# Performance work log

Hardware: AMD Instinct MI355X
Metric: run time of the kernel (lower is better)

## Reference

```python
import jax, jax.numpy as jnp
import numpy as np

HIDDEN = 64
IN_SIZE = 2048 + 512  # sum(obs_shape) + sum(action_shape)


def setup_inputs() -> dict:
    key = jax.random.key(0)
    ks = jax.random.split(key, 10)
    B = 32768
    s_in = 1.0 / np.sqrt(IN_SIZE)
    s_h = 1.0 / np.sqrt(HIDDEN)
    return {
        "state": jax.random.normal(ks[0], (B, 2048), dtype=jnp.float32),
        "action": jax.random.normal(ks[1], (B, 512), dtype=jnp.float32),
        "hidden_state": jax.random.normal(ks[2], (B, HIDDEN), dtype=jnp.float32),
        "cell_state": jax.random.normal(ks[3], (B, HIDDEN), dtype=jnp.float32),
        # fused gate weights, gate order: [i, f, g, o]
        "Wi": jax.random.uniform(ks[4], (IN_SIZE, 4 * HIDDEN), jnp.float32, -s_in, s_in),
        "bi": jax.random.uniform(ks[5], (4 * HIDDEN,), jnp.float32, -s_in, s_in),
        "Wh": jax.random.uniform(ks[6], (HIDDEN, 4 * HIDDEN), jnp.float32, -s_h, s_h),
        "bh": jax.random.uniform(ks[7], (4 * HIDDEN,), jnp.float32, -s_h, s_h),
        "Wo": jax.random.uniform(ks[8], (HIDDEN, 1), jnp.float32, -s_h, s_h),
        "bo": jax.random.uniform(ks[9], (1,), jnp.float32, -s_h, s_h),
    }


def reference(state, action, hidden_state, cell_state, Wi, bi, Wh, bh, Wo, bo):
    x = jnp.concatenate([state, action], axis=1)  # [B, IN_SIZE]
    # two fused GEMMs covering all 8 Linear layers (gate order i,f,g,o)
    gates = x @ Wi + bi + hidden_state @ Wh + bh  # [B, 4*HIDDEN]
    i_t, f_t, g_t, o_t = jnp.split(gates, 4, axis=1)
    i_t = jax.nn.sigmoid(i_t)
    f_t = jax.nn.sigmoid(f_t)
    g_t = jnp.tanh(g_t)
    o_t = jax.nn.sigmoid(o_t)
    c_t = f_t * cell_state + i_t * g_t
    h_t = o_t * jnp.tanh(c_t)
    out = jnp.tanh(h_t @ Wo + bo)  # [B, 1]
    return (out, h_t, c_t)
```

## Files before the change

kernel.cpp:

```cpp
#include <hip/hip_runtime.h>
#include <hip/hip_bf16.h>

#define K_IN 2624
#define NSTEP 82

typedef __attribute__((ext_vector_type(8))) short short8;
typedef __attribute__((ext_vector_type(4))) float float4_t;

__device__ __forceinline__ short f2bf(float f) {
    union { __hip_bfloat16 b; short s; } u;
    u.b = __float2bfloat16(f);
    return u.s;
}

__device__ __forceinline__ float sigmoid_fast(float x) {
    return 1.f / (1.f + __expf(-x));
}

__device__ __forceinline__ float tanh_fast(float x) {
    float e = __expf(-2.f * fabsf(x));
    float t = (1.f - e) / (1.f + e);
    return copysignf(t, x);
}

__global__ void prep_kernel(const float* __restrict__ Wi, const float* __restrict__ bi,
                            const float* __restrict__ Wh, const float* __restrict__ bh,
                            short* __restrict__ Wt2, float* __restrict__ bsum) {
    __shared__ short tile[32][264];
    const int t = threadIdx.x;
    const int kb = blockIdx.x;
    const int k0 = kb * 32;

#pragma unroll 8
    for (int j = 0; j < 32; ++j) {
        int k = k0 + j;
        float v = (k < 2560) ? Wi[(size_t)k * 256 + t]
                             : Wh[(size_t)(k - 2560) * 256 + t];
        tile[j][t] = f2bf(v);
    }
    if (kb == 0) bsum[t] = bi[t] + bh[t];
    __syncthreads();

#pragma unroll
    for (int c = 0; c < 4; ++c) {
        int idx = c * 256 + t;
        int lane = idx & 63;
        int nb = idx >> 6;
        int n = nb * 16 + (lane & 15);
        int j0 = (lane >> 4) * 8;
        short8 v;
#pragma unroll
        for (int j = 0; j < 8; ++j) v[j] = tile[j0 + j][n];
        *reinterpret_cast<short8*>(Wt2 + (size_t)kb * 8192 + (size_t)idx * 8) = v;
    }
}

__global__ __launch_bounds__(64, 2)
void lstm_kernel(const float* __restrict__ state, const float* __restrict__ action,
                 const float* __restrict__ hidden, const float* __restrict__ cell,
                 const short* __restrict__ Wt2, const float* __restrict__ bsum,
                 const float* __restrict__ Wo, const float* __restrict__ bo,
                 float* __restrict__ out, int Brows) {
    __shared__ float sG[16 * 260];

    const int l = threadIdx.x;
    const int bm = blockIdx.x;
    const int lr = l & 15;
    const int q = l >> 4;

    const size_t mrow = (size_t)bm * 16 + lr;
    const float* aS = state  + mrow * 2048 + q * 8;
    const float* aA = action + mrow * 512  + q * 8;
    const float* aH = hidden + mrow * 64   + q * 8;
    const short* bP = Wt2 + (size_t)l * 8;

    float4_t acc[16];
#pragma unroll
    for (int nb = 0; nb < 16; ++nb) acc[nb] = (float4_t)(0.f);

    short8 Bc[16];
    float4_t Ac0, Ac1;
#pragma unroll
    for (int nb = 0; nb < 16; ++nb)
        Bc[nb] = *reinterpret_cast<const short8*>(bP + nb * 512);
    Ac0 = __builtin_nontemporal_load(reinterpret_cast<const float4_t*>(aS));
    Ac1 = __builtin_nontemporal_load(reinterpret_cast<const float4_t*>(aS + 4));

#pragma unroll 2
    for (int s = 0; s < 81; ++s) {
        short8 Bn[16];
        float4_t An0, An1;
        const short* bp1 = bP + (size_t)(s + 1) * 8192;
#pragma unroll
        for (int nb = 0; nb < 16; ++nb)
            Bn[nb] = *reinterpret_cast<const short8*>(bp1 + nb * 512);
        {
            int sn = s + 1;
            const float* p;
            int col;
            if (sn < 64)      { p = aS; col = sn * 32; }
            else if (sn < 80) { p = aA; col = (sn - 64) * 32; }
            else              { p = aH; col = (sn - 80) * 32; }
            An0 = __builtin_nontemporal_load(reinterpret_cast<const float4_t*>(p + col));
            An1 = __builtin_nontemporal_load(reinterpret_cast<const float4_t*>(p + col + 4));
        }

        short8 a;
        a[0] = f2bf(Ac0[0]); a[1] = f2bf(Ac0[1]); a[2] = f2bf(Ac0[2]); a[3] = f2bf(Ac0[3]);
        a[4] = f2bf(Ac1[0]); a[5] = f2bf(Ac1[1]); a[6] = f2bf(Ac1[2]); a[7] = f2bf(Ac1[3]);
#pragma unroll
        for (int nb = 0; nb < 16; ++nb)
            acc[nb] = __builtin_amdgcn_mfma_f32_16x16x32_bf16(a, Bc[nb], acc[nb], 0, 0, 0);

#pragma unroll
        for (int nb = 0; nb < 16; ++nb) Bc[nb] = Bn[nb];
        Ac0 = An0; Ac1 = An1;
    }
    {
        short8 a;
        a[0] = f2bf(Ac0[0]); a[1] = f2bf(Ac0[1]); a[2] = f2bf(Ac0[2]); a[3] = f2bf(Ac0[3]);
        a[4] = f2bf(Ac1[0]); a[5] = f2bf(Ac1[1]); a[6] = f2bf(Ac1[2]); a[7] = f2bf(Ac1[3]);
#pragma unroll
        for (int nb = 0; nb < 16; ++nb)
            acc[nb] = __builtin_amdgcn_mfma_f32_16x16x32_bf16(a, Bc[nb], acc[nb], 0, 0, 0);
    }

#pragma unroll
    for (int nb = 0; nb < 16; ++nb)
#pragma unroll
        for (int r = 0; r < 4; ++r)
            sG[(q * 4 + r) * 260 + nb * 16 + lr] = acc[nb][r];
    __syncthreads();

    const float wo = Wo[l];
    const float bov = bo[0];
    const float b0 = bsum[l];
    const float b1 = bsum[64 + l];
    const float b2 = bsum[128 + l];
    const float b3 = bsum[192 + l];
    float* outH = out + Brows;
    float* outC = outH + (size_t)Brows * 64;

#pragma unroll
    for (int r = 0; r < 16; ++r) {
        size_t grow = (size_t)bm * 16 + r;
        float gi = sG[r * 260 + l]       + b0;
        float gf = sG[r * 260 + 64 + l]  + b1;
        float gg = sG[r * 260 + 128 + l] + b2;
        float go = sG[r * 260 + 192 + l] + b3;
        float i_t = sigmoid_fast(gi);
        float f_t = sigmoid_fast(gf);
        float g_t = tanh_fast(gg);
        float o_t = sigmoid_fast(go);
        float c_t = f_t * cell[grow * 64 + l] + i_t * g_t;
        float h_t = o_t * tanh_fast(c_t);
        outC[grow * 64 + l] = c_t;
        outH[grow * 64 + l] = h_t;
        float v = h_t * wo;
#pragma unroll
        for (int off = 32; off > 0; off >>= 1) v += __shfl_down(v, off);
        if (l == 0) out[grow] = tanh_fast(v + bov);
    }
}

extern "C" void kernel_launch(void* const* d_in, const int* in_sizes, int n_in,
                              void* d_out, int out_size, void* d_ws, size_t ws_size,
                              hipStream_t stream) {
    const float* state  = (const float*)d_in[0];
    const float* action = (const float*)d_in[1];
    const float* hidden = (const float*)d_in[2];
    const float* cell   = (const float*)d_in[3];
    const float* Wi     = (const float*)d_in[4];
    const float* bi     = (const float*)d_in[5];
    const float* Wh     = (const float*)d_in[6];
    const float* bh     = (const float*)d_in[7];
    const float* Wo     = (const float*)d_in[8];
    const float* bo     = (const float*)d_in[9];

    const int Brows = in_sizes[0] / 2048;

    short* Wt2  = (short*)d_ws;
    float* bsum = (float*)((char*)d_ws + (size_t)NSTEP * 8192 * sizeof(short));

    prep_kernel<<<NSTEP, 256, 0, stream>>>(Wi, bi, Wh, bh, Wt2, bsum);
    lstm_kernel<<<Brows / 16, 64, 0, stream>>>(state, action, hidden, cell,
                                               Wt2, bsum, Wo, bo, (float*)d_out, Brows);
}
```

Before: 542.8 us.

## Share weight tiles across four waves via double-buffered LDS staging

Blocks grow from one wave on 16 rows to four waves on 64 rows. Each 2-step weight chunk is loaded cooperatively into a double-buffered LDS tile and read by all four waves, so global/L2 weight traffic per row drops by a factor of four. Activations are prefetched two chunks ahead with regular (non-nontemporal) loads. This adds a block-wide barrier per chunk and 64KB of LDS per block, which may limit occupancy.

```diff
diff --git a/kernel.cpp b/kernel.cpp
--- a/kernel.cpp
+++ b/kernel.cpp
@@ -3,6 +3,7 @@
 
 #define K_IN 2624
 #define NSTEP 82
+#define NCHUNK 41
 
 typedef __attribute__((ext_vector_type(8))) short short8;
 typedef __attribute__((ext_vector_type(4))) float float4_t;
@@ -55,81 +56,97 @@
     }
 }
 
-__global__ __launch_bounds__(64, 2)
+__global__ __launch_bounds__(256, 2)
 void lstm_kernel(const float* __restrict__ state, const float* __restrict__ action,
                  const float* __restrict__ hidden, const float* __restrict__ cell,
                  const short* __restrict__ Wt2, const float* __restrict__ bsum,
                  const float* __restrict__ Wo, const float* __restrict__ bo,
                  float* __restrict__ out, int Brows) {
-    __shared__ float sG[16 * 260];
-
-    const int l = threadIdx.x;
-    const int bm = blockIdx.x;
+    __shared__ __align__(16) short sB[2 * 16384];
+
+    const int t = threadIdx.x;
+    const int w = t >> 6;
+    const int l = t & 63;
     const int lr = l & 15;
     const int q = l >> 4;
-
-    const size_t mrow = (size_t)bm * 16 + lr;
-    const float* aS = state  + mrow * 2048 + q * 8;
-    const float* aA = action + mrow * 512  + q * 8;
-    const float* aH = hidden + mrow * 64   + q * 8;
-    const short* bP = Wt2 + (size_t)l * 8;
+    const int bm = blockIdx.x;
+
+    const size_t mrow = (size_t)bm * 64 + w * 16 + lr;
+    const float* aS = state  + mrow * 2048;
+    const float* aA = action + mrow * 512;
+    const float* aH = hidden + mrow * 64;
+
+    const short* bg = Wt2 + t * 8;
 
     float4_t acc[16];
 #pragma unroll
     for (int nb = 0; nb < 16; ++nb) acc[nb] = (float4_t)(0.f);
 
-    short8 Bc[16];
-    float4_t Ac0, Ac1;
+    float4_t aCur[4], aNxt[4], bReg[8];
+
+    auto loadA = [&](int c, float4_t* dst) {
+        const float* p; int col;
+        if (c < 32)      { p = aS; col = c * 64; }
+        else if (c < 40) { p = aA; col = (c - 32) * 64; }
+        else             { p = aH; col = 0; }
+        dst[0] = *reinterpret_cast<const float4_t*>(p + col + q * 8);
+        dst[1] = *reinterpret_cast<const float4_t*>(p + col + q * 8 + 4);
+        dst[2] = *reinterpret_cast<const float4_t*>(p + col + 32 + q * 8);
+        dst[3] = *reinterpret_cast<const float4_t*>(p + col + 32 + q * 8 + 4);
+    };
+    auto loadB = [&](int c) {
+#pragma unroll
+        for (int i = 0; i < 8; ++i)
+            bReg[i] = *reinterpret_cast<const float4_t*>(bg + (size_t)c * 16384 + i * 2048);
+    };
+    auto storeB = [&](int c) {
+        short* d = sB + (c & 1) * 16384 + t * 8;
+#pragma unroll
+        for (int i = 0; i < 8; ++i)
+            *reinterpret_cast<float4_t*>(d + i * 2048) = bReg[i];
+    };
+
+    loadB(0);
+    loadA(0, aCur);
+    loadA(1, aNxt);
+    storeB(0);
+    __syncthreads();
+
+    for (int k = 0; k < NCHUNK; ++k) {
+        if (k + 1 < NCHUNK) loadB(k + 1);
+
+        const short* bufr = sB + (k & 1) * 16384;
+#pragma unroll
+        for (int s = 0; s < 2; ++s) {
+            short8 a;
+            a[0] = f2bf(aCur[2*s][0]); a[1] = f2bf(aCur[2*s][1]);
+            a[2] = f2bf(aCur[2*s][2]); a[3] = f2bf(aCur[2*s][3]);
+            a[4] = f2bf(aCur[2*s+1][0]); a[5] = f2bf(aCur[2*s+1][1]);
+            a[6] = f2bf(aCur[2*s+1][2]); a[7] = f2bf(aCur[2*s+1][3]);
+#pragma unroll
+            for (int nb = 0; nb < 16; ++nb) {
+                short8 b = *reinterpret_cast<const short8*>(bufr + s * 8192 + nb * 512 + l * 8);
+                acc[nb] = __builtin_amdgcn_mfma_f32_16x16x32_bf16(a, b, acc[nb], 0, 0, 0);
+            }
+        }
+
+#pragma unroll
+        for (int i = 0; i < 4; ++i) aCur[i] = aNxt[i];
+        if (k + 2 < NCHUNK) loadA(k + 2, aNxt);
+
+        if (k + 1 < NCHUNK) {
+            storeB(k + 1);
+            __syncthreads();
+        }
+    }
+
+    __syncthreads();
+    float* sG = reinterpret_cast<float*>(sB) + w * 4096;
 #pragma unroll
     for (int nb = 0; nb < 16; ++nb)
-        Bc[nb] = *reinterpret_cast<const short8*>(bP + nb * 512);
-    Ac0 = __builtin_nontemporal_load(reinterpret_cast<const float4_t*>(aS));
-    Ac1 = __builtin_nontemporal_load(reinterpret_cast<const float4_t*>(aS + 4));
-
-#pragma unroll 2
-    for (int s = 0; s < 81; ++s) {
-        short8 Bn[16];
-        float4_t An0, An1;
-        const short* bp1 = bP + (size_t)(s + 1) * 8192;
-#pragma unroll
-        for (int nb = 0; nb < 16; ++nb)
-            Bn[nb] = *reinterpret_cast<const short8*>(bp1 + nb * 512);
-        {
-            int sn = s + 1;
-            const float* p;
-            int col;
-            if (sn < 64)      { p = aS; col = sn * 32; }
-            else if (sn < 80) { p = aA; col = (sn - 64) * 32; }
-            else              { p = aH; col = (sn - 80) * 32; }
-            An0 = __builtin_nontemporal_load(reinterpret_cast<const float4_t*>(p + col));
-            An1 = __builtin_nontemporal_load(reinterpret_cast<const float4_t*>(p + col + 4));
-        }
-
-        short8 a;
-        a[0] = f2bf(Ac0[0]); a[1] = f2bf(Ac0[1]); a[2] = f2bf(Ac0[2]); a[3] = f2bf(Ac0[3]);
-        a[4] = f2bf(Ac1[0]); a[5] = f2bf(Ac1[1]); a[6] = f2bf(Ac1[2]); a[7] = f2bf(Ac1[3]);
-#pragma unroll
-        for (int nb = 0; nb < 16; ++nb)
-            acc[nb] = __builtin_amdgcn_mfma_f32_16x16x32_bf16(a, Bc[nb], acc[nb], 0, 0, 0);
-
-#pragma unroll
-        for (int nb = 0; nb < 16; ++nb) Bc[nb] = Bn[nb];
-        Ac0 = An0; Ac1 = An1;
-    }
-    {
-        short8 a;
-        a[0] = f2bf(Ac0[0]); a[1] = f2bf(Ac0[1]); a[2] = f2bf(Ac0[2]); a[3] = f2bf(Ac0[3]);
-        a[4] = f2bf(Ac1[0]); a[5] = f2bf(Ac1[1]); a[6] = f2bf(Ac1[2]); a[7] = f2bf(Ac1[3]);
-#pragma unroll
-        for (int nb = 0; nb < 16; ++nb)
-            acc[nb] = __builtin_amdgcn_mfma_f32_16x16x32_bf16(a, Bc[nb], acc[nb], 0, 0, 0);
-    }
-
-#pragma unroll
-    for (int nb = 0; nb < 16; ++nb)
 #pragma unroll
         for (int r = 0; r < 4; ++r)
-            sG[(q * 4 + r) * 260 + nb * 16 + lr] = acc[nb][r];
+            sG[(q * 4 + r) * 256 + nb * 16 + lr] = acc[nb][r];
     __syncthreads();
 
     const float wo = Wo[l];
@@ -143,11 +160,11 @@
 
 #pragma unroll
     for (int r = 0; r < 16; ++r) {
-        size_t grow = (size_t)bm * 16 + r;
-        float gi = sG[r * 260 + l]       + b0;
-        float gf = sG[r * 260 + 64 + l]  + b1;
-        float gg = sG[r * 260 + 128 + l] + b2;
-        float go = sG[r * 260 + 192 + l] + b3;
+        size_t grow = (size_t)bm * 64 + w * 16 + r;
+        float gi = sG[r * 256 + l]       + b0;
+        float gf = sG[r * 256 + 64 + l]  + b1;
+        float gg = sG[r * 256 + 128 + l] + b2;
+        float go = sG[r * 256 + 192 + l] + b3;
         float i_t = sigmoid_fast(gi);
         float f_t = sigmoid_fast(gf);
         float g_t = tanh_fast(gg);
@@ -183,6 +200,6 @@
     float* bsum = (float*)((char*)d_ws + (size_t)NSTEP * 8192 * sizeof(short));
 
     prep_kernel<<<NSTEP, 256, 0, stream>>>(Wi, bi, Wh, bh, Wt2, bsum);
-    lstm_kernel<<<Brows / 16, 64, 0, stream>>>(state, action, hidden, cell,
-                                               Wt2, bsum, Wo, bo, (float*)d_out, Brows);
-}
+    lstm_kernel<<<Brows / 64, 256, 0, stream>>>(state, action, hidden, cell,
+                                                Wt2, bsum, Wo, bo, (float*)d_out, Brows);
+}
```

Result: faster. 460.6 us (-15.1%).

## Share LDS-staged bf16 weight tiles across four waves per 32-row block

Applied to the files above, without the earlier changes.

Replaces the single-wave, 16-row block with a 256-thread block covering 32 rows. Each wave owns 64 gate columns. Weight chunks are double-buffered into LDS via global_load_lds, so one copy serves all four waves. Activations are converted to bf16 into an LDS double buffer that all waves read. This roughly halves per-row weight traffic from L2 and cuts the large per-lane register footprint, at the cost of a block-wide barrier every K step.

```diff
diff --git a/kernel.cpp b/kernel.cpp
--- a/kernel.cpp
+++ b/kernel.cpp
@@ -3,8 +3,10 @@
 
 #define K_IN 2624
 #define NSTEP 82
+#define NCH 82
 
 typedef __attribute__((ext_vector_type(8))) short short8;
+typedef __attribute__((ext_vector_type(4))) short short4_t;
 typedef __attribute__((ext_vector_type(4))) float float4_t;
 
 __device__ __forceinline__ short f2bf(float f) {
@@ -55,81 +57,100 @@
     }
 }
 
-__global__ __launch_bounds__(64, 2)
+__global__ __launch_bounds__(256, 4)
 void lstm_kernel(const float* __restrict__ state, const float* __restrict__ action,
                  const float* __restrict__ hidden, const float* __restrict__ cell,
                  const short* __restrict__ Wt2, const float* __restrict__ bsum,
                  const float* __restrict__ Wo, const float* __restrict__ bo,
                  float* __restrict__ out, int Brows) {
-    __shared__ float sG[16 * 260];
-
-    const int l = threadIdx.x;
-    const int bm = blockIdx.x;
+    __shared__ __align__(16) char smem[36864];
+    short* sB = (short*)smem;
+    short* sA = (short*)(smem + 32768);
+    float* sG = (float*)smem;
+
+    const int t = threadIdx.x;
+    const int w = t >> 6;
+    const int l = t & 63;
     const int lr = l & 15;
     const int q = l >> 4;
-
-    const size_t mrow = (size_t)bm * 16 + lr;
-    const float* aS = state  + mrow * 2048 + q * 8;
-    const float* aA = action + mrow * 512  + q * 8;
-    const float* aH = hidden + mrow * 64   + q * 8;
-    const short* bP = Wt2 + (size_t)l * 8;
-
-    float4_t acc[16];
-#pragma unroll
-    for (int nb = 0; nb < 16; ++nb) acc[nb] = (float4_t)(0.f);
-
-    short8 Bc[16];
-    float4_t Ac0, Ac1;
-#pragma unroll
-    for (int nb = 0; nb < 16; ++nb)
-        Bc[nb] = *reinterpret_cast<const short8*>(bP + nb * 512);
-    Ac0 = __builtin_nontemporal_load(reinterpret_cast<const float4_t*>(aS));
-    Ac1 = __builtin_nontemporal_load(reinterpret_cast<const float4_t*>(aS + 4));
+    const int bm = blockIdx.x;
+
+    const int ar = t >> 3;
+    const int akc = (t & 7) * 4;
+
+    const size_t rowbase = (size_t)bm * 32;
+    const float* aS = state  + (rowbase + ar) * 2048 + akc;
+    const float* aA = action + (rowbase + ar) * 512  + akc;
+    const float* aH = hidden + (rowbase + ar) * 64   + akc;
+
+    float4_t acc[2][4];
+#pragma unroll
+    for (int mt = 0; mt < 2; ++mt)
+#pragma unroll
+        for (int nt = 0; nt < 4; ++nt) acc[mt][nt] = (float4_t)(0.f);
+
+    auto loadA = [&](int c) -> float4_t {
+        const float* p;
+        if (c < 64)      p = aS + c * 32;
+        else if (c < 80) p = aA + (c - 64) * 32;
+        else             p = aH + (c - 80) * 32;
+        return __builtin_nontemporal_load(reinterpret_cast<const float4_t*>(p));
+    };
+    auto writeA = [&](int slot, float4_t v) {
+        short4_t s4;
+        s4[0] = f2bf(v[0]); s4[1] = f2bf(v[1]); s4[2] = f2bf(v[2]); s4[3] = f2bf(v[3]);
+        *reinterpret_cast<short4_t*>(sA + slot * 1024 + ar * 32 + akc) = s4;
+    };
+    auto stageB = [&](int c) {
+        const int slot = c & 1;
+#pragma unroll
+        for (int i = 0; i < 4; ++i) {
+            int blk = w * 4 + i;
+            __builtin_amdgcn_global_load_lds(
+                (const __attribute__((address_space(1))) void*)(Wt2 + (size_t)c * 8192 + blk * 512 + l * 8),
+                (__attribute__((address_space(3))) void*)(sB + slot * 8192 + blk * 512),
+                16, 0, 0);
+        }
+    };
+
+    float4_t aG[2];
+
+    stageB(0);
+    aG[0] = loadA(0);
+    aG[1] = loadA(1);
+    writeA(0, aG[0]);
+    __syncthreads();
 
 #pragma unroll 2
-    for (int s = 0; s < 81; ++s) {
-        short8 Bn[16];
-        float4_t An0, An1;
-        const short* bp1 = bP + (size_t)(s + 1) * 8192;
-#pragma unroll
-        for (int nb = 0; nb < 16; ++nb)
-            Bn[nb] = *reinterpret_cast<const short8*>(bp1 + nb * 512);
-        {
-            int sn = s + 1;
-            const float* p;
-            int col;
-            if (sn < 64)      { p = aS; col = sn * 32; }
-            else if (sn < 80) { p = aA; col = (sn - 64) * 32; }
-            else              { p = aH; col = (sn - 80) * 32; }
-            An0 = __builtin_nontemporal_load(reinterpret_cast<const float4_t*>(p + col));
-            An1 = __builtin_nontemporal_load(reinterpret_cast<const float4_t*>(p + col + 4));
-        }
-
-        short8 a;
-        a[0] = f2bf(Ac0[0]); a[1] = f2bf(Ac0[1]); a[2] = f2bf(Ac0[2]); a[3] = f2bf(Ac0[3]);
-        a[4] = f2bf(Ac1[0]); a[5] = f2bf(Ac1[1]); a[6] = f2bf(Ac1[2]); a[7] = f2bf(Ac1[3]);
-#pragma unroll
-        for (int nb = 0; nb < 16; ++nb)
-            acc[nb] = __builtin_amdgcn_mfma_f32_16x16x32_bf16(a, Bc[nb], acc[nb], 0, 0, 0);
-
-#pragma unroll
-        for (int nb = 0; nb < 16; ++nb) Bc[nb] = Bn[nb];
-        Ac0 = An0; Ac1 = An1;
-    }
-    {
-        short8 a;
-        a[0] = f2bf(Ac0[0]); a[1] = f2bf(Ac0[1]); a[2] = f2bf(Ac0[2]); a[3] = f2bf(Ac0[3]);
-        a[4] = f2bf(Ac1[0]); a[5] = f2bf(Ac1[1]); a[6] = f2bf(Ac1[2]); a[7] = f2bf(Ac1[3]);
-#pragma unroll
-        for (int nb = 0; nb < 16; ++nb)
-            acc[nb] = __builtin_amdgcn_mfma_f32_16x16x32_bf16(a, Bc[nb], acc[nb], 0, 0, 0);
-    }
-
-#pragma unroll
-    for (int nb = 0; nb < 16; ++nb)
-#pragma unroll
-        for (int r = 0; r < 4; ++r)
-            sG[(q * 4 + r) * 260 + nb * 16 + lr] = acc[nb][r];
+    for (int k = 0; k < NCH; ++k) {
+        const int slot = k & 1;
+        if (k + 1 < NCH) stageB(k + 1);
+        if (k + 2 < NCH) aG[k & 1] = loadA(k + 2);
+
+        short8 a0 = *reinterpret_cast<const short8*>(sA + slot * 1024 + lr * 32 + q * 8);
+        short8 a1 = *reinterpret_cast<const short8*>(sA + slot * 1024 + (16 + lr) * 32 + q * 8);
+        short8 b[4];
+#pragma unroll
+        for (int nt = 0; nt < 4; ++nt)
+            b[nt] = *reinterpret_cast<const short8*>(sB + slot * 8192 + (w * 4 + nt) * 512 + l * 8);
+#pragma unroll
+        for (int nt = 0; nt < 4; ++nt)
+            acc[0][nt] = __builtin_amdgcn_mfma_f32_16x16x32_bf16(a0, b[nt], acc[0][nt], 0, 0, 0);
+#pragma unroll
+        for (int nt = 0; nt < 4; ++nt)
+            acc[1][nt] = __builtin_amdgcn_mfma_f32_16x16x32_bf16(a1, b[nt], acc[1][nt], 0, 0, 0);
+
+        if (k + 1 < NCH) writeA((k + 1) & 1, aG[(k + 1) & 1]);
+        __syncthreads();
+    }
+
+#pragma unroll
+    for (int mt = 0; mt < 2; ++mt)
+#pragma unroll
+        for (int nt = 0; nt < 4; ++nt)
+#pragma unroll
+            for (int r = 0; r < 4; ++r)
+                sG[(mt * 16 + q * 4 + r) * 260 + w * 64 + nt * 16 + lr] = acc[mt][nt][r];
     __syncthreads();
 
     const float wo = Wo[l];
@@ -142,12 +163,13 @@
     float* outC = outH + (size_t)Brows * 64;
 
 #pragma unroll
-    for (int r = 0; r < 16; ++r) {
-        size_t grow = (size_t)bm * 16 + r;
-        float gi = sG[r * 260 + l]       + b0;
-        float gf = sG[r * 260 + 64 + l]  + b1;
-        float gg = sG[r * 260 + 128 + l] + b2;
-        float go = sG[r * 260 + 192 + l] + b3;
+    for (int r = 0; r < 8; ++r) {
+        int rr = w * 8 + r;
+        size_t grow = rowbase + rr;
+        float gi = sG[rr * 260 + l]       + b0;
+        float gf = sG[rr * 260 + 64 + l]  + b1;
+        float gg = sG[rr * 260 + 128 + l] + b2;
+        float go = sG[rr * 260 + 192 + l] + b3;
         float i_t = sigmoid_fast(gi);
         float f_t = sigmoid_fast(gf);
         float g_t = tanh_fast(gg);
@@ -183,6 +205,6 @@
     float* bsum = (float*)((char*)d_ws + (size_t)NSTEP * 8192 * sizeof(short));
 
     prep_kernel<<<NSTEP, 256, 0, stream>>>(Wi, bi, Wh, bh, Wt2, bsum);
-    lstm_kernel<<<Brows / 16, 64, 0, stream>>>(state, action, hidden, cell,
-                                               Wt2, bsum, Wo, bo, (float*)d_out, Brows);
-}
+    lstm_kernel<<<Brows / 32, 256, 0, stream>>>(state, action, hidden, cell,
+                                                Wt2, bsum, Wo, bo, (float*)d_out, Brows);
+}
```

New measurement: 470.8 us. -13.2%, faster.
